# Optimization experiments

Measured on AMD Instinct MI355X. Metric: run time of the kernel, lower is better.

## Reference

```python
import jax, jax.numpy as jnp
import numpy as np

N_NODES = 50000
N_EDGES = 1600000
IN_DIM = 128
HEADS = 4
HEAD_DIM = 32  # out_dim // heads
N_REL = 3
NEG_SLOPE = 0.2


def setup_inputs() -> dict:
    key = jax.random.key(0)
    ks = jax.random.split(key, 8)
    x = jax.random.normal(ks[0], (N_NODES, IN_DIM), dtype=jnp.float32)
    edge_index = jax.random.randint(ks[1], (2, N_EDGES), 0, N_NODES, dtype=jnp.int64)
    edge_type = jax.random.randint(ks[2], (N_EDGES,), 0, N_REL, dtype=jnp.int64)
    # per-relation GATConv params (PyG layout: lin weight, att_src, att_dst, bias)
    s = 1.0 / np.sqrt(IN_DIM)
    W = jax.random.normal(ks[3], (N_REL, IN_DIM, HEADS * HEAD_DIM), dtype=jnp.float32) * s
    att_src = jax.random.normal(ks[4], (N_REL, HEADS, HEAD_DIM), dtype=jnp.float32) * s
    att_dst = jax.random.normal(ks[5], (N_REL, HEADS, HEAD_DIM), dtype=jnp.float32) * s
    bias = jnp.zeros((N_REL, HEADS * HEAD_DIM), dtype=jnp.float32)
    rel_w = jnp.ones((N_REL,), dtype=jnp.float32)  # relation_weights param
    return {"x": x, "W": W, "att_src": att_src, "att_dst": att_dst,
            "bias": bias, "rel_w": rel_w,
            "edge_index": edge_index, "edge_type": edge_type}


def reference(x, W, att_src, att_dst, bias, rel_w, edge_index, edge_type):
    N = x.shape[0]
    NEG = jnp.float32(-1e9)
    # self loops (GATConv add_self_loops=True) appended; present in every relation
    self_idx = jnp.arange(N, dtype=edge_index.dtype)
    src = jnp.concatenate([edge_index[0], self_idx])  # [E+N]
    dst = jnp.concatenate([edge_index[1], self_idx])  # [E+N]
    weights = jax.nn.softmax(rel_w)
    out = jnp.zeros((N, HEADS * HEAD_DIM), dtype=x.dtype)
    for r in range(N_REL):
        h = (x @ W[r]).reshape(N, HEADS, HEAD_DIM)  # [N,H,C]
        a_s = jnp.einsum('nhc,hc->nh', h, att_src[r])
        a_d = jnp.einsum('nhc,hc->nh', h, att_dst[r])
        score = jax.nn.leaky_relu(a_s[src] + a_d[dst], NEG_SLOPE)  # [E+N,H]
        mask = jnp.concatenate([edge_type == r, jnp.ones((N,), dtype=bool)])
        score = jnp.where(mask[:, None], score, NEG)  # mask out other relations
        # segment softmax over incoming edges per destination node
        smax = jax.ops.segment_max(score, dst, num_segments=N)  # finite: self-loops
        ex = jnp.exp(score - smax[dst])
        denom = jax.ops.segment_sum(ex, dst, num_segments=N)
        alpha = ex / denom[dst]  # [E+N,H]
        msg = alpha[:, :, None] * h[src]  # [E+N,H,C]
        rel_out = jax.ops.segment_sum(msg, dst, num_segments=N).reshape(N, HEADS * HEAD_DIM)
        out = out + weights[r] * (rel_out + bias[r])
    return out
```

## Files before the change

### kernel.cpp

```cpp
#include <hip/hip_runtime.h>
#include <hip/hip_bf16.h>
#include <hip/hip_fp16.h>
#include <math.h>

#define IN_DIM 128
#define OUT_DIM 128
#define HEADS 4
#define HEAD_DIM 32
#define NREL 3
#define NEG_SLOPE 0.2f

#define CHUNK 4096
#define BUCK_SHIFT 7
#define DPB 128
#define KPB 384
#define CAPE 6144
#define CAPS (CAPE + 3*DPB)

typedef __attribute__((ext_vector_type(8))) short short8;
typedef __attribute__((ext_vector_type(4))) float f32x4;
typedef unsigned short u16;

static __device__ __forceinline__ float leaky(float x){ return fmaxf(x, NEG_SLOPE*x); }
static __device__ __forceinline__ unsigned bf16rn(float x){
  unsigned b = __float_as_uint(x);
  b += 0x7FFF + ((b>>16)&1u);
  return b>>16;
}
static __device__ __forceinline__ unsigned h2pack(float a, float b){
  union { __half h[2]; unsigned u; } p;
  p.h[0] = __float2half_rn(a); p.h[1] = __float2half_rn(b);
  return p.u;
}

__global__ __launch_bounds__(256) void k_wprep(
    const float* __restrict__ W, const float* __restrict__ att_s,
    const float* __restrict__ att_d, const float* __restrict__ rw,
    const float* __restrict__ bias, u16* __restrict__ WTall,
    float* __restrict__ smw, float* __restrict__ biasMix){
  const int r = blockIdx.x / 9;
  const int tile = blockIdx.x % 9;
  const int t = threadIdx.x;
  const float* Wr = W + (size_t)r*IN_DIM*OUT_DIM;
  u16* WT = WTall + (size_t)r*144*128;
  if (tile < 8){
    const int col0 = tile*16;
    for (int i=t; i<16*128; i+=256){
      int col = col0 + (i>>7), k = i&127;
      WT[col*128 + k] = (u16)bf16rn(Wr[k*128 + col]);
    }
    return;
  }
  if (t < 128){
    int k = t;
    for (int h=0; h<4; h++){
      float ss=0.f, sd=0.f;
      for (int c=0; c<32; c++){
        float w = Wr[k*128 + h*32 + c];
        ss = fmaf(w, att_s[(r*4+h)*32+c], ss);
        sd = fmaf(w, att_d[(r*4+h)*32+c], sd);
      }
      WT[(128+h)*128 + k] = (u16)bf16rn(ss);
      WT[(132+h)*128 + k] = (u16)bf16rn(sd);
    }
  }
  for (int i=t; i<8*128; i+=256) WT[136*128 + i] = 0;
  if (r == 0){
    float m = fmaxf(rw[0], fmaxf(rw[1], rw[2]));
    float e0=__expf(rw[0]-m), e1=__expf(rw[1]-m), e2=__expf(rw[2]-m);
    float inv = 1.f/(e0+e1+e2);
    if (t < 3) smw[t] = (t==0?e0:(t==1?e1:e2))*inv;
    if (t < 128)
      biasMix[t] = inv*(e0*bias[t] + e1*bias[OUT_DIM+t] + e2*bias[2*OUT_DIM+t]);
  }
}

__global__ __launch_bounds__(256) void k_gemmhist(
    const float* __restrict__ x, const u16* __restrict__ WTall,
    unsigned* __restrict__ hq, float* __restrict__ as_, float* __restrict__ ad_,
    const int* __restrict__ ei, int* __restrict__ histG,
    int N, int E, int NCHUNK, int NBUCK){
  __shared__ u16 lds16[128][136];
  const int t = threadIdx.x;

  if (blockIdx.x < (unsigned)NCHUNK){
    int* h = (int*)&lds16[0][0];
    const int c = blockIdx.x;
    h[t] = 0; h[t+256] = 0; __syncthreads();
    const int* dstp = ei + E;
    const int base = c*CHUNK;
    #pragma unroll 4
    for (int it=0; it<CHUNK/256; ++it){
      int e = base + it*256 + t;
      if (e < E) atomicAdd(&h[dstp[e]>>BUCK_SHIFT], 1);
    }
    __syncthreads();
    for (int k=t; k<NBUCK; k+=256) histG[c*NBUCK + k] = h[k];
    return;
  }

  const int w = t >> 6;
  const int l = t & 63;
  const int blkrow0 = (blockIdx.x - NCHUNK)*128;
  const int row0 = blkrow0 + w*32;
  const int lg = l >> 4;
  const int lc = l & 15;

  short8 afrag[4][2];
  #pragma unroll
  for (int ks=0; ks<4; ks++){
    const int k0 = ks*32 + lg*8;
    #pragma unroll
    for (int rf=0; rf<2; rf++){
      int row = row0 + rf*16 + lc;
      float4 v0, v1;
      if (row < N){
        const float4* xp = (const float4*)(x + (size_t)row*IN_DIM + k0);
        v0 = xp[0]; v1 = xp[1];
      } else { v0 = float4{0.f,0.f,0.f,0.f}; v1 = v0; }
      union { short8 s; unsigned u[4]; } pa;
      pa.u[0] = bf16rn(v0.x) | (bf16rn(v0.y)<<16);
      pa.u[1] = bf16rn(v0.z) | (bf16rn(v0.w)<<16);
      pa.u[2] = bf16rn(v1.x) | (bf16rn(v1.y)<<16);
      pa.u[3] = bf16rn(v1.z) | (bf16rn(v1.w)<<16);
      afrag[ks][rf] = pa.s;
    }
  }

  for (int r=0; r<NREL; r++){
    const u16* WT = WTall + (size_t)r*144*128;
    f32x4 acc[2][9];
    #pragma unroll
    for (int rf=0; rf<2; rf++)
      #pragma unroll
      for (int cf=0; cf<9; cf++) acc[rf][cf] = (f32x4){0.f,0.f,0.f,0.f};

    #pragma unroll
    for (int ks=0; ks<4; ks++){
      const int k0 = ks*32 + lg*8;
      #pragma unroll
      for (int cf=0; cf<9; cf++){
        short8 b = *(const short8*)(WT + (size_t)(cf*16 + lc)*128 + k0);
        #pragma unroll
        for (int rf=0; rf<2; rf++)
          acc[rf][cf] = __builtin_amdgcn_mfma_f32_16x16x32_bf16(afrag[ks][rf], b, acc[rf][cf], 0, 0, 0);
      }
    }

    __syncthreads();
    #pragma unroll
    for (int rf=0; rf<2; rf++){
      #pragma unroll
      for (int j=0; j<4; j++){
        const int rloc = w*32 + rf*16 + lg*4 + j;
        #pragma unroll
        for (int cf=0; cf<8; cf++)
          lds16[rloc][cf*16 + lc] = (u16)bf16rn(acc[rf][cf][j]);
        int row = row0 + rf*16 + lg*4 + j;
        float av = acc[rf][8][j];
        if (row < N){
          size_t nidx = (size_t)r*N + row;
          if (lc < 4)       as_[nidx*4 + lc]     = av;
          else if (lc < 8)  ad_[nidx*4 + (lc-4)] = av;
        }
      }
    }
    __syncthreads();
    #pragma unroll
    for (int k=0; k<8; k++){
      int i = t + 256*k;
      int row = i >> 4, q = i & 15;
      int grow = blkrow0 + row;
      if (grow < N){
        size_t nidx = (size_t)r*N + grow;
        *(uint4*)(hq + nidx*64 + q*4) = *(const uint4*)&lds16[row][q*8];
      }
    }
  }
}

__global__ __launch_bounds__(256) void k_scanSeg(const int* __restrict__ histG,
                        int* __restrict__ chunkOff, int* __restrict__ totalE,
                        int NCHUNK, int NBUCK){
  __shared__ int sh[512];
  __shared__ int ps[256];
  const int b = blockIdx.x, t = threadIdx.x;
  sh[t]     = (t     < NCHUNK) ? histG[(size_t)t*NBUCK + b]       : 0;
  sh[t+256] = (t+256 < NCHUNK) ? histG[(size_t)(t+256)*NBUCK + b] : 0;
  __syncthreads();
  int e0 = sh[2*t], pair = e0 + sh[2*t+1];
  ps[t] = pair; __syncthreads();
  int x = pair;
  for (int off=1; off<256; off<<=1){
    int y = (t>=off)?ps[t-off]:0; __syncthreads();
    x += y; ps[t] = x; __syncthreads();
  }
  int ex = x - pair;
  if (2*t   < NCHUNK) chunkOff[(size_t)(2*t)*NBUCK + b]   = ex;
  if (2*t+1 < NCHUNK) chunkOff[(size_t)(2*t+1)*NBUCK + b] = ex + e0;
  if (t == 255) totalE[b] = x;
}

__global__ __launch_bounds__(256) void k_part(const int* __restrict__ et, const int* __restrict__ ei,
                       const int* __restrict__ chunkOff, unsigned* __restrict__ payload,
                       int E, int NCHUNK, int NBUCK){
  __shared__ int cur[512];
  const int c = blockIdx.x, t = threadIdx.x;
  for (int k=t; k<NBUCK; k+=256) cur[k] = k*CAPE + chunkOff[(size_t)c*NBUCK + k];
  __syncthreads();
  const int* dstp = ei + E;
  const int base = c*CHUNK;
  #pragma unroll 4
  for (int it=0; it<CHUNK/256; ++it){
    int e = base + it*256 + t;
    if (e < E){
      int d = dstp[e];
      int s = ei[e];
      int r = et[e];
      int b = d >> BUCK_SHIFT;
      int pos = atomicAdd(&cur[b], 1);
      payload[pos] = (unsigned)((d & (DPB-1)) | (r<<7) | (s<<9));
    }
  }
}

__global__ __launch_bounds__(512) void k_csr(const unsigned* __restrict__ payload,
                     const int* __restrict__ totalE,
                     const float* __restrict__ as_, const float* __restrict__ ad_,
                     const float* __restrict__ smw,
                     int* __restrict__ offs, uint4* __restrict__ slot,
                     float4* __restrict__ ivg,
                     int E, int N, int NCHUNK, int NBUCK){
  __shared__ unsigned shp[CAPE];
  __shared__ int cntA[KPB];
  __shared__ int cur[KPB];
  __shared__ float den[KPB*4];
  __shared__ float4 adl[KPB];
  __shared__ int wtot[2];
  const int b = blockIdx.x, t = threadIdx.x;
  const int bs = b*CAPE;
  const int ne = totalE[b];
  const int outbase = b*CAPS;
  const int validD = min(N - b*DPB, DPB);

  for (int k=t; k<KPB; k+=512) cntA[k] = 0;
  for (int k=t; k<KPB*4; k+=512) den[k] = 0.f;
  for (int k=t; k<KPB; k+=512){
    int dl = k/3, r = k - dl*3;
    int d2 = b*DPB + dl;
    adl[k] = (d2 < N) ? ((const float4*)ad_)[(size_t)r*N + d2] : (float4){0,0,0,0};
  }
  __syncthreads();
  for (int i=t; i<ne; i+=512){
    unsigned p = payload[bs + i];
    shp[i] = p;
    atomicAdd(&cntA[(int)(p&(DPB-1))*NREL + (int)((p>>7)&3u)], 1);
  }
  __syncthreads();
  const int dst = b*DPB + t;
  int c0=0,c1=0,c2=0,sum=0,o0=0,o1=0,o2=0,hs=0,xinc=0;
  if (t < DPB){
    hs = (dst < N) ? 1 : 0;
    c0 = cntA[3*t]   + hs;
    c1 = cntA[3*t+1] + hs;
    c2 = cntA[3*t+2] + hs;
    sum = c0+c1+c2;
    xinc = sum;
    #pragma unroll
    for (int o=1; o<64; o<<=1){
      int y = __shfl_up(xinc, o);
      if ((t & 63) >= o) xinc += y;
    }
    if ((t & 63) == 63) wtot[t>>6] = xinc;
  }
  __syncthreads();
  if (t < DPB){
    int ex = xinc - sum + ((t >= 64) ? wtot[0] : 0);
    o0 = outbase + ex; o1 = o0 + c0; o2 = o1 + c1;
    offs[b*(KPB+1) + 3*t]   = o0;
    offs[b*(KPB+1) + 3*t+1] = o1;
    offs[b*(KPB+1) + 3*t+2] = o2;
    cur[3*t]   = (o0 - outbase) + hs;
    cur[3*t+1] = (o1 - outbase) + hs;
    cur[3*t+2] = (o2 - outbase) + hs;
  }
  if (t == 0) offs[b*(KPB+1) + KPB] = outbase + ne + 3*validD;
  __syncthreads();
  for (int i=t; i<ne; i+=512){
    unsigned p = shp[i];
    int dl = (int)(p&(DPB-1)), r = (int)((p>>7)&3u), s = (int)(p>>9);
    int lkey = dl*NREL + r;
    int pos = outbase + atomicAdd(&cur[lkey], 1);
    float4 a4 = ((const float4*)as_)[(size_t)r*N + s];
    float4 b4 = adl[lkey];
    float ex0 = __expf(leaky(a4.x+b4.x));
    float ex1 = __expf(leaky(a4.y+b4.y));
    float ex2 = __expf(leaky(a4.z+b4.z));
    float ex3 = __expf(leaky(a4.w+b4.w));
    slot[pos] = (uint4){ (unsigned)(s | (r<<16)), h2pack(ex0,ex1), h2pack(ex2,ex3), 0u };
    atomicAdd(&den[lkey*4+0], ex0); atomicAdd(&den[lkey*4+1], ex1);
    atomicAdd(&den[lkey*4+2], ex2); atomicAdd(&den[lkey*4+3], ex3);
  }
  __syncthreads();
  if (t < DPB && dst < N){
    int starts[3] = {o0, o1, o2};
    #pragma unroll
    for (int r=0; r<NREL; r++){
      int lkey = 3*t + r;
      float4 a4 = ((const float4*)as_)[(size_t)r*N + dst];
      float4 b4 = adl[lkey];
      float s0 = __expf(leaky(a4.x+b4.x));
      float s1 = __expf(leaky(a4.y+b4.y));
      float s2 = __expf(leaky(a4.z+b4.z));
      float s3 = __expf(leaky(a4.w+b4.w));
      float w = smw[r];
      float4 iv;
      iv.x = w/(den[lkey*4+0]+s0);
      iv.y = w/(den[lkey*4+1]+s1);
      iv.z = w/(den[lkey*4+2]+s2);
      iv.w = w/(den[lkey*4+3]+s3);
      ivg[dst*3 + r] = iv;
      slot[starts[r]] = (uint4){ (unsigned)(dst | (r<<16)), h2pack(s0,s1), h2pack(s2,s3), 0u };
    }
  }
}

__global__ __launch_bounds__(128) void k_segment(
    const int* __restrict__ offs, const uint4* __restrict__ slot,
    const unsigned* __restrict__ hq,
    const float4* __restrict__ ivg, const float* __restrict__ biasMix,
    float* __restrict__ out, int N){
  const int wave = threadIdx.x >> 6;
  const int lane = threadIdx.x & 63;
  const int dst  = blockIdx.x*2 + wave;
  if (dst >= N) return;
  const int g  = lane >> 3;
  const int l8 = lane & 7;
  const int h0 = l8 >> 2;

  const int bb = dst >> BUCK_SHIFT;
  const int lk = (dst & (DPB-1))*3;
  const int* ob = offs + (size_t)bb*(KPB+1);
  int beg = __builtin_amdgcn_readfirstlane(ob[lk]);
  int end = __builtin_amdgcn_readfirstlane(ob[lk+3]);

  float4 v0 = ivg[dst*3+0], v1 = ivg[dst*3+1], v2 = ivg[dst*3+2];
  float iA0 = h0 ? v0.y : v0.x, iB0 = h0 ? v0.w : v0.z;
  float iA1 = h0 ? v1.y : v1.x, iB1 = h0 ? v1.w : v1.z;
  float iA2 = h0 ? v2.y : v2.x, iB2 = h0 ? v2.w : v2.z;

  float acc0[8], acc1[8];
  #pragma unroll
  for (int q=0; q<8; q++){ acc0[q]=0.f; acc1[q]=0.f; }

  for (int i0=beg; i0<end; i0+=16){
    int i = i0 + g;
    int j = i + 8;
    bool vi = (i < end), vj = (j < end);
    uint4 rec1 = {0,0,0,0}, rec2 = {0,0,0,0};
    if (vi) rec1 = slot[i];
    if (vj) rec2 = slot[j];
    uint4 u0a, u1a, u0b, u1b;
    if (vi){
      int s = (int)(rec1.x & 0xFFFFu);
      int r = (int)((rec1.x >> 16) & 3u);
      const uint4* hp = (const uint4*)(hq + ((size_t)r*N + s)*64 + l8*4);
      u0a = hp[0]; u1a = hp[8];
    }
    if (vj){
      int s = (int)(rec2.x & 0xFFFFu);
      int r = (int)((rec2.x >> 16) & 3u);
      const uint4* hp = (const uint4*)(hq + ((size_t)r*N + s)*64 + l8*4);
      u0b = hp[0]; u1b = hp[8];
    }
    if (vi){
      int r = (int)((rec1.x >> 16) & 3u);
      float ivA = (r==0)? iA0 : (r==1)? iA1 : iA2;
      float ivB = (r==0)? iB0 : (r==1)? iB1 : iB2;
      union { unsigned u; __half h[2]; } pa, pb;
      pa.u = rec1.y; pb.u = rec1.z;
      float a0 = __half2float(pa.h[h0]) * ivA;
      float a1 = __half2float(pb.h[h0]) * ivB;
      const unsigned* p0 = (const unsigned*)&u0a;
      const unsigned* p1 = (const unsigned*)&u1a;
      #pragma unroll
      for (int q=0; q<4; q++){
        acc0[2*q]   = fmaf(a0, __uint_as_float(p0[q]<<16),           acc0[2*q]);
        acc0[2*q+1] = fmaf(a0, __uint_as_float(p0[q] & 0xFFFF0000u), acc0[2*q+1]);
        acc1[2*q]   = fmaf(a1, __uint_as_float(p1[q]<<16),           acc1[2*q]);
        acc1[2*q+1] = fmaf(a1, __uint_as_float(p1[q] & 0xFFFF0000u), acc1[2*q+1]);
      }
    }
    if (vj){
      int r = (int)((rec2.x >> 16) & 3u);
      float ivA = (r==0)? iA0 : (r==1)? iA1 : iA2;
      float ivB = (r==0)? iB0 : (r==1)? iB1 : iB2;
      union { unsigned u; __half h[2]; } pa, pb;
      pa.u = rec2.y; pb.u = rec2.z;
      float a0 = __half2float(pa.h[h0]) * ivA;
      float a1 = __half2float(pb.h[h0]) * ivB;
      const unsigned* p0 = (const unsigned*)&u0b;
      const unsigned* p1 = (const unsigned*)&u1b;
      #pragma unroll
      for (int q=0; q<4; q++){
        acc0[2*q]   = fmaf(a0, __uint_as_float(p0[q]<<16),           acc0[2*q]);
        acc0[2*q+1] = fmaf(a0, __uint_as_float(p0[q] & 0xFFFF0000u), acc0[2*q+1]);
        acc1[2*q]   = fmaf(a1, __uint_as_float(p1[q]<<16),           acc1[2*q]);
        acc1[2*q+1] = fmaf(a1, __uint_as_float(p1[q] & 0xFFFF0000u), acc1[2*q+1]);
      }
    }
  }

  #pragma unroll
  for (int o=8; o<=32; o<<=1){
    #pragma unroll
    for (int q=0; q<8; q++){
      acc0[q] += __shfl_xor(acc0[q], o);
      acc1[q] += __shfl_xor(acc1[q], o);
    }
  }

  if (g == 0){
    const float4* bmA = (const float4*)(biasMix + 8*l8);
    const float4* bmB = (const float4*)(biasMix + 64 + 8*l8);
    float4 x0 = bmA[0], x1 = bmA[1], y0 = bmB[0], y1 = bmB[1];
    float* orow = out + (size_t)dst*OUT_DIM;
    float4 o0 = {acc0[0]+x0.x, acc0[1]+x0.y, acc0[2]+x0.z, acc0[3]+x0.w};
    float4 o1 = {acc0[4]+x1.x, acc0[5]+x1.y, acc0[6]+x1.z, acc0[7]+x1.w};
    float4 o2 = {acc1[0]+y0.x, acc1[1]+y0.y, acc1[2]+y0.z, acc1[3]+y0.w};
    float4 o3 = {acc1[4]+y1.x, acc1[5]+y1.y, acc1[6]+y1.z, acc1[7]+y1.w};
    *(float4*)(orow + 8*l8)          = o0;
    *(float4*)(orow + 8*l8 + 4)      = o1;
    *(float4*)(orow + 64 + 8*l8)     = o2;
    *(float4*)(orow + 64 + 8*l8 + 4) = o3;
  }
}

extern "C" void kernel_launch(void* const* d_in, const int* in_sizes, int n_in,
                              void* d_out, int out_size, void* d_ws, size_t ws_size,
                              hipStream_t stream) {
  const float* x     = (const float*)d_in[0];
  const float* W     = (const float*)d_in[1];
  const float* att_s = (const float*)d_in[2];
  const float* att_d = (const float*)d_in[3];
  const float* bias  = (const float*)d_in[4];
  const float* rw    = (const float*)d_in[5];
  const int*   ei    = (const int*)d_in[6];
  const int*   et    = (const int*)d_in[7];
  float* out = (float*)d_out;

  const int N = in_sizes[0] / IN_DIM;
  const int E = in_sizes[7];
  const int M = NREL * N;
  const int NCHUNK = (E + CHUNK - 1) / CHUNK;
  const int NBUCK  = (N + DPB - 1) / DPB;
  const int GB     = (N + 127) / 128;

  char* ws = (char*)d_ws;
  size_t off = 0;
  auto alloc = [&](size_t bytes) -> void* {
    void* p = ws + off; off += (bytes + 255) & ~(size_t)255; return p;
  };
  unsigned* hq       = (unsigned*)alloc((size_t)M * 64 * 4);
  float*    as_      = (float*)   alloc((size_t)M * 4 * 4);
  float*    ad_      = (float*)   alloc((size_t)M * 4 * 4);
  int*      offs     = (int*)     alloc((size_t)NBUCK * (KPB+1) * 4);
  int*      histG    = (int*)     alloc((size_t)NBUCK * NCHUNK * 4);
  int*      chunkOff = (int*)     alloc((size_t)NBUCK * NCHUNK * 4);
  int*      totalE   = (int*)     alloc((size_t)NBUCK * 4);
  unsigned* payload  = (unsigned*)alloc((size_t)NBUCK * CAPE * 4);
  uint4*    slot     = (uint4*)   alloc((size_t)NBUCK * CAPS * 16);
  float4*   ivg      = (float4*)  alloc((size_t)M * 16);
  float*    smw      = (float*)   alloc(256);
  float*    biasMix  = (float*)   alloc(512);
  u16*      WTall    = (u16*)     alloc((size_t)NREL * 144 * 128 * 2);

  k_wprep<<<NREL*9, 256, 0, stream>>>(W, att_s, att_d, rw, bias, WTall, smw, biasMix);
  k_gemmhist<<<NCHUNK + GB, 256, 0, stream>>>(x, WTall, hq, as_, ad_, ei, histG, N, E, NCHUNK, NBUCK);
  k_scanSeg<<<NBUCK, 256, 0, stream>>>(histG, chunkOff, totalE, NCHUNK, NBUCK);
  k_part<<<NCHUNK, 256, 0, stream>>>(et, ei, chunkOff, payload, E, NCHUNK, NBUCK);
  k_csr<<<NBUCK, 512, 0, stream>>>(payload, totalE, as_, ad_, smw, offs, slot, ivg, E, N, NCHUNK, NBUCK);
  k_segment<<<(N + 1) / 2, 128, 0, stream>>>(offs, slot, hq, ivg, biasMix, out, N);
}
```

Baseline: 200.3 us.

## Split projection GEMM: compute scores early, co-schedule hq GEMM with CSR build

The first kernel now computes only the attention-score columns (as/ad) next to the histogram, which shortens the critical path before the scan and partition stages. The full 128-column projection that writes hq moves into a merged kernel that runs alongside the CSR/softmax-denominator blocks, so the GEMM overlaps with the bucket CSR work. Shared memory is a union of both roles. In exchange, x is read twice and the GEMM blocks use 16 rows per wave with 512 threads, which may change occupancy. The merged kernel's LDS footprint is set by the CSR layout.

```diff
diff --git a/kernel.cpp b/kernel.cpp
--- a/kernel.cpp
+++ b/kernel.cpp
@@ -75,34 +75,32 @@
   }
 }
 
-__global__ __launch_bounds__(256) void k_gemmhist(
+__global__ __launch_bounds__(512) void k_prep2(
     const float* __restrict__ x, const u16* __restrict__ WTall,
-    unsigned* __restrict__ hq, float* __restrict__ as_, float* __restrict__ ad_,
+    float* __restrict__ as_, float* __restrict__ ad_,
     const int* __restrict__ ei, int* __restrict__ histG,
     int N, int E, int NCHUNK, int NBUCK){
-  __shared__ u16 lds16[128][136];
+  __shared__ int h[512];
   const int t = threadIdx.x;
 
   if (blockIdx.x < (unsigned)NCHUNK){
-    int* h = (int*)&lds16[0][0];
     const int c = blockIdx.x;
-    h[t] = 0; h[t+256] = 0; __syncthreads();
+    h[t] = 0; __syncthreads();
     const int* dstp = ei + E;
     const int base = c*CHUNK;
     #pragma unroll 4
-    for (int it=0; it<CHUNK/256; ++it){
-      int e = base + it*256 + t;
+    for (int it=0; it<CHUNK/512; ++it){
+      int e = base + it*512 + t;
       if (e < E) atomicAdd(&h[dstp[e]>>BUCK_SHIFT], 1);
     }
     __syncthreads();
-    for (int k=t; k<NBUCK; k+=256) histG[c*NBUCK + k] = h[k];
+    for (int k=t; k<NBUCK; k+=512) histG[c*NBUCK + k] = h[k];
     return;
   }
 
   const int w = t >> 6;
   const int l = t & 63;
-  const int blkrow0 = (blockIdx.x - NCHUNK)*128;
-  const int row0 = blkrow0 + w*32;
+  const int row0 = (blockIdx.x - NCHUNK)*256 + w*32;
   const int lg = l >> 4;
   const int lc = l & 15;
 
@@ -129,51 +127,28 @@
 
   for (int r=0; r<NREL; r++){
     const u16* WT = WTall + (size_t)r*144*128;
-    f32x4 acc[2][9];
-    #pragma unroll
-    for (int rf=0; rf<2; rf++)
-      #pragma unroll
-      for (int cf=0; cf<9; cf++) acc[rf][cf] = (f32x4){0.f,0.f,0.f,0.f};
-
+    f32x4 acc[2];
+    acc[0] = (f32x4){0.f,0.f,0.f,0.f};
+    acc[1] = (f32x4){0.f,0.f,0.f,0.f};
     #pragma unroll
     for (int ks=0; ks<4; ks++){
       const int k0 = ks*32 + lg*8;
-      #pragma unroll
-      for (int cf=0; cf<9; cf++){
-        short8 b = *(const short8*)(WT + (size_t)(cf*16 + lc)*128 + k0);
-        #pragma unroll
-        for (int rf=0; rf<2; rf++)
-          acc[rf][cf] = __builtin_amdgcn_mfma_f32_16x16x32_bf16(afrag[ks][rf], b, acc[rf][cf], 0, 0, 0);
-      }
-    }
-
-    __syncthreads();
+      short8 b = *(const short8*)(WT + (size_t)(128 + lc)*128 + k0);
+      #pragma unroll
+      for (int rf=0; rf<2; rf++)
+        acc[rf] = __builtin_amdgcn_mfma_f32_16x16x32_bf16(afrag[ks][rf], b, acc[rf], 0, 0, 0);
+    }
     #pragma unroll
     for (int rf=0; rf<2; rf++){
       #pragma unroll
       for (int j=0; j<4; j++){
-        const int rloc = w*32 + rf*16 + lg*4 + j;
-        #pragma unroll
-        for (int cf=0; cf<8; cf++)
-          lds16[rloc][cf*16 + lc] = (u16)bf16rn(acc[rf][cf][j]);
         int row = row0 + rf*16 + lg*4 + j;
-        float av = acc[rf][8][j];
         if (row < N){
           size_t nidx = (size_t)r*N + row;
+          float av = acc[rf][j];
           if (lc < 4)       as_[nidx*4 + lc]     = av;
           else if (lc < 8)  ad_[nidx*4 + (lc-4)] = av;
         }
-      }
-    }
-    __syncthreads();
-    #pragma unroll
-    for (int k=0; k<8; k++){
-      int i = t + 256*k;
-      int row = i >> 4, q = i & 15;
-      int grow = blkrow0 + row;
-      if (grow < N){
-        size_t nidx = (size_t)r*N + grow;
-        *(uint4*)(hq + nidx*64 + q*4) = *(const uint4*)&lds16[row][q*8];
       }
     }
   }
@@ -224,103 +199,177 @@
   }
 }
 
-__global__ __launch_bounds__(512) void k_csr(const unsigned* __restrict__ payload,
-                     const int* __restrict__ totalE,
-                     const float* __restrict__ as_, const float* __restrict__ ad_,
-                     const float* __restrict__ smw,
-                     int* __restrict__ offs, uint4* __restrict__ slot,
-                     float4* __restrict__ ivg,
-                     int E, int N, int NCHUNK, int NBUCK){
-  __shared__ unsigned shp[CAPE];
-  __shared__ int cntA[KPB];
-  __shared__ int cur[KPB];
-  __shared__ float den[KPB*4];
-  __shared__ float4 adl[KPB];
-  __shared__ int wtot[2];
-  const int b = blockIdx.x, t = threadIdx.x;
-  const int bs = b*CAPE;
-  const int ne = totalE[b];
-  const int outbase = b*CAPS;
-  const int validD = min(N - b*DPB, DPB);
-
-  for (int k=t; k<KPB; k+=512) cntA[k] = 0;
-  for (int k=t; k<KPB*4; k+=512) den[k] = 0.f;
-  for (int k=t; k<KPB; k+=512){
-    int dl = k/3, r = k - dl*3;
-    int d2 = b*DPB + dl;
-    adl[k] = (d2 < N) ? ((const float4*)ad_)[(size_t)r*N + d2] : (float4){0,0,0,0};
-  }
-  __syncthreads();
-  for (int i=t; i<ne; i+=512){
-    unsigned p = payload[bs + i];
-    shp[i] = p;
-    atomicAdd(&cntA[(int)(p&(DPB-1))*NREL + (int)((p>>7)&3u)], 1);
-  }
-  __syncthreads();
-  const int dst = b*DPB + t;
-  int c0=0,c1=0,c2=0,sum=0,o0=0,o1=0,o2=0,hs=0,xinc=0;
-  if (t < DPB){
-    hs = (dst < N) ? 1 : 0;
-    c0 = cntA[3*t]   + hs;
-    c1 = cntA[3*t+1] + hs;
-    c2 = cntA[3*t+2] + hs;
-    sum = c0+c1+c2;
-    xinc = sum;
-    #pragma unroll
-    for (int o=1; o<64; o<<=1){
-      int y = __shfl_up(xinc, o);
-      if ((t & 63) >= o) xinc += y;
-    }
-    if ((t & 63) == 63) wtot[t>>6] = xinc;
-  }
-  __syncthreads();
-  if (t < DPB){
-    int ex = xinc - sum + ((t >= 64) ? wtot[0] : 0);
-    o0 = outbase + ex; o1 = o0 + c0; o2 = o1 + c1;
-    offs[b*(KPB+1) + 3*t]   = o0;
-    offs[b*(KPB+1) + 3*t+1] = o1;
-    offs[b*(KPB+1) + 3*t+2] = o2;
-    cur[3*t]   = (o0 - outbase) + hs;
-    cur[3*t+1] = (o1 - outbase) + hs;
-    cur[3*t+2] = (o2 - outbase) + hs;
-  }
-  if (t == 0) offs[b*(KPB+1) + KPB] = outbase + ne + 3*validD;
-  __syncthreads();
-  for (int i=t; i<ne; i+=512){
-    unsigned p = shp[i];
-    int dl = (int)(p&(DPB-1)), r = (int)((p>>7)&3u), s = (int)(p>>9);
-    int lkey = dl*NREL + r;
-    int pos = outbase + atomicAdd(&cur[lkey], 1);
-    float4 a4 = ((const float4*)as_)[(size_t)r*N + s];
-    float4 b4 = adl[lkey];
-    float ex0 = __expf(leaky(a4.x+b4.x));
-    float ex1 = __expf(leaky(a4.y+b4.y));
-    float ex2 = __expf(leaky(a4.z+b4.z));
-    float ex3 = __expf(leaky(a4.w+b4.w));
-    slot[pos] = (uint4){ (unsigned)(s | (r<<16)), h2pack(ex0,ex1), h2pack(ex2,ex3), 0u };
-    atomicAdd(&den[lkey*4+0], ex0); atomicAdd(&den[lkey*4+1], ex1);
-    atomicAdd(&den[lkey*4+2], ex2); atomicAdd(&den[lkey*4+3], ex3);
-  }
-  __syncthreads();
-  if (t < DPB && dst < N){
-    int starts[3] = {o0, o1, o2};
-    #pragma unroll
-    for (int r=0; r<NREL; r++){
-      int lkey = 3*t + r;
-      float4 a4 = ((const float4*)as_)[(size_t)r*N + dst];
-      float4 b4 = adl[lkey];
-      float s0 = __expf(leaky(a4.x+b4.x));
-      float s1 = __expf(leaky(a4.y+b4.y));
-      float s2 = __expf(leaky(a4.z+b4.z));
-      float s3 = __expf(leaky(a4.w+b4.w));
-      float w = smw[r];
-      float4 iv;
-      iv.x = w/(den[lkey*4+0]+s0);
-      iv.y = w/(den[lkey*4+1]+s1);
-      iv.z = w/(den[lkey*4+2]+s2);
-      iv.w = w/(den[lkey*4+3]+s3);
-      ivg[dst*3 + r] = iv;
-      slot[starts[r]] = (uint4){ (unsigned)(dst | (r<<16)), h2pack(s0,s1), h2pack(s2,s3), 0u };
+__global__ __launch_bounds__(512) void k_mega(
+    const unsigned* __restrict__ payload, const int* __restrict__ totalE,
+    const float* __restrict__ as_, const float* __restrict__ ad_,
+    const float* __restrict__ smw,
+    int* __restrict__ offs, uint4* __restrict__ slot, float4* __restrict__ ivg,
+    const float* __restrict__ x, const u16* __restrict__ WTall,
+    unsigned* __restrict__ hq,
+    int E, int N, int NBUCK){
+  union SMem {
+    struct {
+      float4 adl[KPB];
+      unsigned shp[CAPE];
+      int cntA[KPB];
+      int cur[KPB];
+      float den[KPB*4];
+      int wtot[2];
+    } c;
+    u16 lds16[128][136];
+  };
+  __shared__ SMem sm;
+  const int t = threadIdx.x;
+
+  if (blockIdx.x < (unsigned)NBUCK){
+    const int b = blockIdx.x;
+    const int bs = b*CAPE;
+    const int ne = totalE[b];
+    const int outbase = b*CAPS;
+    const int validD = min(N - b*DPB, DPB);
+
+    for (int k=t; k<KPB; k+=512) sm.c.cntA[k] = 0;
+    for (int k=t; k<KPB*4; k+=512) sm.c.den[k] = 0.f;
+    for (int k=t; k<KPB; k+=512){
+      int dl = k/3, r = k - dl*3;
+      int d2 = b*DPB + dl;
+      sm.c.adl[k] = (d2 < N) ? ((const float4*)ad_)[(size_t)r*N + d2] : (float4){0,0,0,0};
+    }
+    __syncthreads();
+    for (int i=t; i<ne; i+=512){
+      unsigned p = payload[bs + i];
+      sm.c.shp[i] = p;
+      atomicAdd(&sm.c.cntA[(int)(p&(DPB-1))*NREL + (int)((p>>7)&3u)], 1);
+    }
+    __syncthreads();
+    const int dst = b*DPB + t;
+    int c0=0,c1=0,c2=0,sum=0,o0=0,o1=0,o2=0,hs=0,xinc=0;
+    if (t < DPB){
+      hs = (dst < N) ? 1 : 0;
+      c0 = sm.c.cntA[3*t]   + hs;
+      c1 = sm.c.cntA[3*t+1] + hs;
+      c2 = sm.c.cntA[3*t+2] + hs;
+      sum = c0+c1+c2;
+      xinc = sum;
+      #pragma unroll
+      for (int o=1; o<64; o<<=1){
+        int y = __shfl_up(xinc, o);
+        if ((t & 63) >= o) xinc += y;
+      }
+      if ((t & 63) == 63) sm.c.wtot[t>>6] = xinc;
+    }
+    __syncthreads();
+    if (t < DPB){
+      int ex = xinc - sum + ((t >= 64) ? sm.c.wtot[0] : 0);
+      o0 = outbase + ex; o1 = o0 + c0; o2 = o1 + c1;
+      offs[b*(KPB+1) + 3*t]   = o0;
+      offs[b*(KPB+1) + 3*t+1] = o1;
+      offs[b*(KPB+1) + 3*t+2] = o2;
+      sm.c.cur[3*t]   = (o0 - outbase) + hs;
+      sm.c.cur[3*t+1] = (o1 - outbase) + hs;
+      sm.c.cur[3*t+2] = (o2 - outbase) + hs;
+    }
+    if (t == 0) offs[b*(KPB+1) + KPB] = outbase + ne + 3*validD;
+    __syncthreads();
+    for (int i=t; i<ne; i+=512){
+      unsigned p = sm.c.shp[i];
+      int dl = (int)(p&(DPB-1)), r = (int)((p>>7)&3u), s = (int)(p>>9);
+      int lkey = dl*NREL + r;
+      int pos = outbase + atomicAdd(&sm.c.cur[lkey], 1);
+      float4 a4 = ((const float4*)as_)[(size_t)r*N + s];
+      float4 b4 = sm.c.adl[lkey];
+      float ex0 = __expf(leaky(a4.x+b4.x));
+      float ex1 = __expf(leaky(a4.y+b4.y));
+      float ex2 = __expf(leaky(a4.z+b4.z));
+      float ex3 = __expf(leaky(a4.w+b4.w));
+      slot[pos] = (uint4){ (unsigned)(s | (r<<16)), h2pack(ex0,ex1), h2pack(ex2,ex3), 0u };
+      atomicAdd(&sm.c.den[lkey*4+0], ex0); atomicAdd(&sm.c.den[lkey*4+1], ex1);
+      atomicAdd(&sm.c.den[lkey*4+2], ex2); atomicAdd(&sm.c.den[lkey*4+3], ex3);
+    }
+    __syncthreads();
+    if (t < DPB && dst < N){
+      int starts[3] = {o0, o1, o2};
+      #pragma unroll
+      for (int r=0; r<NREL; r++){
+        int lkey = 3*t + r;
+        float4 a4 = ((const float4*)as_)[(size_t)r*N + dst];
+        float4 b4 = sm.c.adl[lkey];
+        float s0 = __expf(leaky(a4.x+b4.x));
+        float s1 = __expf(leaky(a4.y+b4.y));
+        float s2 = __expf(leaky(a4.z+b4.z));
+        float s3 = __expf(leaky(a4.w+b4.w));
+        float w = smw[r];
+        float4 iv;
+        iv.x = w/(sm.c.den[lkey*4+0]+s0);
+        iv.y = w/(sm.c.den[lkey*4+1]+s1);
+        iv.z = w/(sm.c.den[lkey*4+2]+s2);
+        iv.w = w/(sm.c.den[lkey*4+3]+s3);
+        ivg[dst*3 + r] = iv;
+        slot[starts[r]] = (uint4){ (unsigned)(dst | (r<<16)), h2pack(s0,s1), h2pack(s2,s3), 0u };
+      }
+    }
+    return;
+  }
+
+  const int w = t >> 6;
+  const int l = t & 63;
+  const int blkrow0 = (blockIdx.x - NBUCK)*128;
+  const int row0 = blkrow0 + w*16;
+  const int lg = l >> 4;
+  const int lc = l & 15;
+
+  short8 afrag[4];
+  #pragma unroll
+  for (int ks=0; ks<4; ks++){
+    const int k0 = ks*32 + lg*8;
+    int row = row0 + lc;
+    float4 v0, v1;
+    if (row < N){
+      const float4* xp = (const float4*)(x + (size_t)row*IN_DIM + k0);
+      v0 = xp[0]; v1 = xp[1];
+    } else { v0 = float4{0.f,0.f,0.f,0.f}; v1 = v0; }
+    union { short8 s; unsigned u[4]; } pa;
+    pa.u[0] = bf16rn(v0.x) | (bf16rn(v0.y)<<16);
+    pa.u[1] = bf16rn(v0.z) | (bf16rn(v0.w)<<16);
+    pa.u[2] = bf16rn(v1.x) | (bf16rn(v1.y)<<16);
+    pa.u[3] = bf16rn(v1.z) | (bf16rn(v1.w)<<16);
+    afrag[ks] = pa.s;
+  }
+
+  for (int r=0; r<NREL; r++){
+    const u16* WT = WTall + (size_t)r*144*128;
+    f32x4 acc[8];
+    #pragma unroll
+    for (int cf=0; cf<8; cf++) acc[cf] = (f32x4){0.f,0.f,0.f,0.f};
+
+    #pragma unroll
+    for (int ks=0; ks<4; ks++){
+      const int k0 = ks*32 + lg*8;
+      #pragma unroll
+      for (int cf=0; cf<8; cf++){
+        short8 b = *(const short8*)(WT + (size_t)(cf*16 + lc)*128 + k0);
+        acc[cf] = __builtin_amdgcn_mfma_f32_16x16x32_bf16(afrag[ks], b, acc[cf], 0, 0, 0);
+      }
+    }
+
+    __syncthreads();
+    #pragma unroll
+    for (int j=0; j<4; j++){
+      const int rloc = w*16 + lg*4 + j;
+      #pragma unroll
+      for (int cf=0; cf<8; cf++)
+        sm.lds16[rloc][cf*16 + lc] = (u16)bf16rn(acc[cf][j]);
+    }
+    __syncthreads();
+    #pragma unroll
+    for (int k=0; k<4; k++){
+      int i = t + 512*k;
+      int row = i >> 4, q = i & 15;
+      int grow = blkrow0 + row;
+      if (grow < N){
+        size_t nidx = (size_t)r*N + grow;
+        *(uint4*)(hq + nidx*64 + q*4) = *(const uint4*)&sm.lds16[row][q*8];
+      }
     }
   }
 }
@@ -454,7 +503,8 @@
   const int M = NREL * N;
   const int NCHUNK = (E + CHUNK - 1) / CHUNK;
   const int NBUCK  = (N + DPB - 1) / DPB;
-  const int GB     = (N + 127) / 128;
+  const int GB2    = (N + 255) / 256;
+  const int GBH    = (N + 127) / 128;
 
   char* ws = (char*)d_ws;
   size_t off = 0;
@@ -476,9 +526,10 @@
   u16*      WTall    = (u16*)     alloc((size_t)NREL * 144 * 128 * 2);
 
   k_wprep<<<NREL*9, 256, 0, stream>>>(W, att_s, att_d, rw, bias, WTall, smw, biasMix);
-  k_gemmhist<<<NCHUNK + GB, 256, 0, stream>>>(x, WTall, hq, as_, ad_, ei, histG, N, E, NCHUNK, NBUCK);
+  k_prep2<<<NCHUNK + GB2, 512, 0, stream>>>(x, WTall, as_, ad_, ei, histG, N, E, NCHUNK, NBUCK);
   k_scanSeg<<<NBUCK, 256, 0, stream>>>(histG, chunkOff, totalE, NCHUNK, NBUCK);
   k_part<<<NCHUNK, 256, 0, stream>>>(et, ei, chunkOff, payload, E, NCHUNK, NBUCK);
-  k_csr<<<NBUCK, 512, 0, stream>>>(payload, totalE, as_, ad_, smw, offs, slot, ivg, E, N, NCHUNK, NBUCK);
+  k_mega<<<NBUCK + GBH, 512, 0, stream>>>(payload, totalE, as_, ad_, smw, offs, slot, ivg,
+                                          x, WTall, hq, E, N, NBUCK);
   k_segment<<<(N + 1) / 2, 128, 0, stream>>>(offs, slot, hq, ivg, biasMix, out, N);
 }
```

After: 209.0 us. 4.3% more time.
